# Kernel optimization log

Hardware: AMD Instinct MI355X
Metric: run time of the kernel (lower is better)

The kernel has to match this reference:

```python
import jax, jax.numpy as jnp
import numpy as np

DIM = 1536
DEPTH = 8
HEADS = 8
KV_HEADS = 1
GROUPS = HEADS // KV_HEADS
DQK = 128
DV = 192
DIM_PW = 128
POOL = 16
FF_INNER = int(DIM * 2.0)
SOFTCLAMP = 5.0
SCALE = 64 ** -0.5  # source uses default dim_head=64 for scale, not dim_head_qk
MAX_POS = 8192
EPS = float(jnp.finfo(jnp.float32).eps)


def rmsnorm(x, g):
    return x * jax.lax.rsqrt(jnp.mean(x * x, axis=-1, keepdims=True) + EPS) * g


def rotate_half(x):
    x1, x2 = jnp.split(x, 2, axis=-1)
    return jnp.concatenate([-x2, x1], axis=-1)


def apply_rope(pos, t):
    return t * jnp.cos(pos) + rotate_half(t) * jnp.sin(pos)


def rotary_emb(seq_len):
    nf = DQK // 2
    # torch.logspace(1, MAX_POS-nf+1, nf) = 10**linspace -> overflows to inf in fp32 (faithful)
    inv_freq = 1.0 / (jnp.arange(nf, dtype=jnp.float32) + 10.0 ** jnp.linspace(1.0, MAX_POS - nf + 1, nf, dtype=jnp.float32))
    freqs = jnp.arange(seq_len, dtype=jnp.float32)[:, None] * inv_freq[None, :]
    return jnp.concatenate([freqs, freqs], axis=-1)  # [n, DQK]


def softclamp(t, value=SOFTCLAMP):
    return jnp.tanh(t / value) * value


def attention(x, pairwise, rope, w_qkv, qg, kg, vg, bg, w_bias, w_out):
    b, n, _ = x.shape
    qkv = x @ w_qkv
    q, k, v = jnp.split(qkv, [HEADS * DQK, HEADS * DQK + DQK], axis=-1)
    # b n (g h d) -> b g h n d
    q = q.reshape(b, n, GROUPS, KV_HEADS, DQK).transpose(0, 2, 3, 1, 4)
    k = k.reshape(b, n, KV_HEADS, DQK).transpose(0, 2, 1, 3)
    v = v.reshape(b, n, KV_HEADS, DV).transpose(0, 2, 1, 3)
    q = rmsnorm(q, qg)
    k = rmsnorm(k, kg)
    v = rmsnorm(v, vg)
    q = q * SCALE
    q = apply_rope(rope, q)
    k = apply_rope(rope, k)
    sim = jnp.einsum('bghid,bhjd->bghij', q, k)
    # pairwise bias: RMSNorm -> GELU -> Linear(dim_pw, heads) -> b g h i j
    pb = jax.nn.gelu(rmsnorm(pairwise, bg), approximate=False) @ w_bias  # [b, i, j, heads]
    bi = pb.shape[1]
    bias = pb.reshape(b, bi, bi, GROUPS, KV_HEADS).transpose(0, 3, 4, 1, 2)
    bias = jnp.repeat(jnp.repeat(bias, POOL, axis=3), POOL, axis=4)  # expand to seq res
    sim = softclamp(sim + bias)
    attn = jax.nn.softmax(sim, axis=-1)
    out = jnp.einsum('bghij,bhjd->bghid', attn, v)
    out = out.transpose(0, 3, 1, 2, 4).reshape(b, n, GROUPS * KV_HEADS * DV)
    return out @ w_out


def tower(x, pairwise, w_qkv, q_gamma, k_gamma, v_gamma, bias_gamma, w_bias, w_out, attn_pre_gamma, ff_pre_gamma, w_ff1, b_ff1, w_ff2, b_ff2):
    rope = rotary_emb(x.shape[1])
    for d in range(DEPTH):
        xn = rmsnorm(x, attn_pre_gamma[d])
        x = x + attention(xn, pairwise, rope, w_qkv[d], q_gamma[d], k_gamma[d], v_gamma[d], bias_gamma[d], w_bias[d], w_out[d])
        xn = rmsnorm(x, ff_pre_gamma[d])
        x = x + (jax.nn.relu(xn @ w_ff1[d] + b_ff1[d]) @ w_ff2[d] + b_ff2[d])
    return x


def setup_inputs() -> dict:
    key = jax.random.key(0)
    ks = jax.random.split(key, 10)
    s = 0.02
    inp = {
        'x': jax.random.normal(ks[0], (2, 2048, DIM), jnp.float32),
        'pairwise': jax.random.normal(ks[1], (2, 128, 128, DIM_PW), jnp.float32),
        'w_qkv': jax.random.normal(ks[2], (DEPTH, DIM, HEADS * DQK + DQK + DV), jnp.float32) * s,
        'q_gamma': jnp.ones((DEPTH, DQK), jnp.float32),
        'k_gamma': jnp.ones((DEPTH, DQK), jnp.float32),
        'v_gamma': jnp.ones((DEPTH, DV), jnp.float32),
        'bias_gamma': jnp.ones((DEPTH, DIM_PW), jnp.float32),
        'w_bias': jax.random.normal(ks[3], (DEPTH, DIM_PW, HEADS), jnp.float32) * s,
        'w_out': jax.random.normal(ks[4], (DEPTH, DV * HEADS, DIM), jnp.float32) * s,
        'attn_pre_gamma': jnp.ones((DEPTH, DIM), jnp.float32),
        'ff_pre_gamma': jnp.ones((DEPTH, DIM), jnp.float32),
        'w_ff1': jax.random.normal(ks[5], (DEPTH, DIM, FF_INNER), jnp.float32) * s,
        'b_ff1': jnp.zeros((DEPTH, FF_INNER), jnp.float32),
        'w_ff2': jax.random.normal(ks[6], (DEPTH, FF_INNER, DIM), jnp.float32) * s,
        'b_ff2': jnp.zeros((DEPTH, DIM), jnp.float32),
    }
    return inp


def reference(x, pairwise, w_qkv, q_gamma, k_gamma, v_gamma, bias_gamma, w_bias, w_out, attn_pre_gamma, ff_pre_gamma, w_ff1, b_ff1, w_ff2, b_ff2):
    return tower(x, pairwise, w_qkv, q_gamma, k_gamma, v_gamma, bias_gamma, w_bias, w_out, attn_pre_gamma, ff_pre_gamma, w_ff1, b_ff1, w_ff2, b_ff2)
```

## Files before the change

kernel.cpp:

```cpp
#include <hip/hip_runtime.h>

typedef __bf16 bf16;
typedef float f32x4 __attribute__((ext_vector_type(4)));
typedef __bf16 bf16x8 __attribute__((ext_vector_type(8)));
typedef __bf16 bf16x4 __attribute__((ext_vector_type(4)));

#define EPSF 1.1920928955078125e-07f

#define GLOAD_LDS16(gsrc, ldst) \
  __builtin_amdgcn_global_load_lds((const __attribute__((address_space(1))) void*)(gsrc), \
                                   (__attribute__((address_space(3))) void*)(ldst), 16, 0, 0)

__device__ __forceinline__ float wave_reduce_sum(float v) {
#pragma unroll
  for (int m = 1; m < 64; m <<= 1) v += __shfl_xor(v, m, 64);
  return v;
}

__global__ __launch_bounds__(256) void wcast_t(const float* __restrict__ src,
                                               bf16* __restrict__ dst, int R, int C) {
  __shared__ float t[32][33];
  int z = blockIdx.z;
  const float* s = src + (size_t)z * R * C;
  bf16* d = dst + (size_t)z * R * C;
  int c0 = blockIdx.x * 32, r0 = blockIdx.y * 32;
  int tx = threadIdx.x, ty = threadIdx.y;
#pragma unroll
  for (int k = 0; k < 4; ++k)
    t[ty + k * 8][tx] = s[(size_t)(r0 + ty + k * 8) * C + c0 + tx];
  __syncthreads();
#pragma unroll
  for (int k = 0; k < 4; ++k)
    d[(size_t)(c0 + ty + k * 8) * R + r0 + tx] = (bf16)t[tx][ty + k * 8];
}

__global__ __launch_bounds__(256) void rmsnorm_k(const float* __restrict__ X,
                                                 const float* __restrict__ G,
                                                 bf16* __restrict__ O) {
  int row = blockIdx.x, tid = threadIdx.x, lane = tid & 63, w = tid >> 6;
  const float* x = X + (size_t)row * 1536;
  float v[6];
  float ss = 0.f;
#pragma unroll
  for (int k = 0; k < 6; ++k) { v[k] = x[tid + k * 256]; ss += v[k] * v[k]; }
  ss = wave_reduce_sum(ss);
  __shared__ float wsum[4];
  if (lane == 0) wsum[w] = ss;
  __syncthreads();
  ss = wsum[0] + wsum[1] + wsum[2] + wsum[3];
  float rs = rsqrtf(ss * (1.f / 1536.f) + EPSF);
  bf16* o = O + (size_t)row * 1536;
#pragma unroll
  for (int k = 0; k < 6; ++k) o[tid + k * 256] = (bf16)(v[k] * rs * G[tid + k * 256]);
}

template <int EPI>
__global__ __launch_bounds__(256, 3) void gemm_bt(const bf16* __restrict__ A,
                                                  const bf16* __restrict__ Bt,
                                                  float* __restrict__ Cf,
                                                  bf16* __restrict__ Cb,
                                                  const float* __restrict__ bias,
                                                  int M, int N, int K) {
  __shared__ __align__(16) char As[128 * 128];
  __shared__ __align__(16) char Bs[128 * 128];
  const int tid = threadIdx.x;
  const int lane = tid & 63, l15 = lane & 15, l4 = lane >> 4;
  const int w = tid >> 6;
  const int nwg = gridDim.x * gridDim.y;
  const int bid = blockIdx.y * gridDim.x + blockIdx.x;
  const int cpx = nwg >> 3;
  const int swz = (bid & 7) * cpx + (bid >> 3);
  const int rm = (swz / gridDim.x) * 128;
  const int cn = (swz % gridDim.x) * 128;
  const int wm = (w >> 1) * 64, wn = (w & 1) * 64;
  f32x4 acc[4][4] = {};

  for (int kk = 0; kk < K; kk += 64) {
#pragma unroll
    for (int r = 0; r < 4; ++r) {
      uint32_t o = (uint32_t)(r * 256 + tid) * 16;
      uint32_t row = o >> 7;
      uint32_t kb = ((o >> 4) & 7) ^ (row & 7);
      const bf16* src = A + (size_t)(rm + (int)row) * K + kk + kb * 8;
      GLOAD_LDS16(src, As + (o & 0xFFFFFC00u));
    }
#pragma unroll
    for (int r = 0; r < 4; ++r) {
      uint32_t o = (uint32_t)(r * 256 + tid) * 16;
      uint32_t row = o >> 7;
      uint32_t kb = ((o >> 4) & 7) ^ (row & 7);
      int nrow = cn + (int)row;
      if (nrow >= N) nrow = N - 1;
      const bf16* src = Bt + (size_t)nrow * K + kk + kb * 8;
      GLOAD_LDS16(src, Bs + (o & 0xFFFFFC00u));
    }
    __syncthreads();
#pragma unroll
    for (int s = 0; s < 2; ++s) {
      bf16x8 a[4], b[4];
#pragma unroll
      for (int m = 0; m < 4; ++m) {
        uint32_t row = wm + m * 16 + l15;
        uint32_t kb = (uint32_t)(s * 4 + l4);
        a[m] = *(const bf16x8*)(As + row * 128 + (kb ^ (row & 7)) * 16);
      }
#pragma unroll
      for (int n = 0; n < 4; ++n) {
        uint32_t row = wn + n * 16 + l15;
        uint32_t kb = (uint32_t)(s * 4 + l4);
        b[n] = *(const bf16x8*)(Bs + row * 128 + (kb ^ (row & 7)) * 16);
      }
      __builtin_amdgcn_s_setprio(1);
#pragma unroll
      for (int m = 0; m < 4; ++m)
#pragma unroll
        for (int n = 0; n < 4; ++n)
          acc[m][n] = __builtin_amdgcn_mfma_f32_16x16x32_bf16(a[m], b[n], acc[m][n], 0, 0, 0);
      __builtin_amdgcn_s_setprio(0);
    }
    __syncthreads();
  }

#pragma unroll
  for (int m = 0; m < 4; ++m)
#pragma unroll
    for (int n = 0; n < 4; ++n)
#pragma unroll
      for (int r = 0; r < 4; ++r) {
        int row = rm + wm + m * 16 + l4 * 4 + r;
        int col = cn + wn + n * 16 + l15;
        if (col < N) {
          float v = acc[m][n][r];
          size_t idx = (size_t)row * N + col;
          if constexpr (EPI == 0) {
            Cf[idx] = v;
          } else if constexpr (EPI == 2) {
            Cf[idx] += v;
          } else if constexpr (EPI == 3) {
            float tv = v + bias[col];
            Cb[idx] = (bf16)(tv > 0.f ? tv : 0.f);
          } else if constexpr (EPI == 4) {
            Cf[idx] += v + bias[col];
          }
        }
      }
}

template <int EPI>
__global__ __launch_bounds__(256, 4) void gemm_bt64(const bf16* __restrict__ A,
                                                    const bf16* __restrict__ Bt,
                                                    float* __restrict__ Cf,
                                                    bf16* __restrict__ Cb,
                                                    const float* __restrict__ bias,
                                                    int M, int N, int K) {
  __shared__ __align__(16) char As[64 * 128];
  __shared__ __align__(16) char Bs[128 * 128];
  const int tid = threadIdx.x;
  const int lane = tid & 63, l15 = lane & 15, l4 = lane >> 4;
  const int w = tid >> 6;
  const int nwg = gridDim.x * gridDim.y;
  const int bid = blockIdx.y * gridDim.x + blockIdx.x;
  const int cpx = nwg >> 3;
  const int swz = (bid & 7) * cpx + (bid >> 3);
  const int rm = (swz / gridDim.x) * 64;
  const int cn = (swz % gridDim.x) * 128;
  const int wm = (w >> 1) * 32, wn = (w & 1) * 64;
  f32x4 acc[2][4] = {};

  for (int kk = 0; kk < K; kk += 64) {
#pragma unroll
    for (int r = 0; r < 2; ++r) {
      uint32_t o = (uint32_t)(r * 256 + tid) * 16;
      uint32_t row = o >> 7;
      uint32_t kb = ((o >> 4) & 7) ^ (row & 7);
      const bf16* src = A + (size_t)(rm + (int)row) * K + kk + kb * 8;
      GLOAD_LDS16(src, As + (o & 0xFFFFFC00u));
    }
#pragma unroll
    for (int r = 0; r < 4; ++r) {
      uint32_t o = (uint32_t)(r * 256 + tid) * 16;
      uint32_t row = o >> 7;
      uint32_t kb = ((o >> 4) & 7) ^ (row & 7);
      int nrow = cn + (int)row;
      if (nrow >= N) nrow = N - 1;
      const bf16* src = Bt + (size_t)nrow * K + kk + kb * 8;
      GLOAD_LDS16(src, Bs + (o & 0xFFFFFC00u));
    }
    __syncthreads();
#pragma unroll
    for (int s = 0; s < 2; ++s) {
      bf16x8 a[2], b[4];
#pragma unroll
      for (int m = 0; m < 2; ++m) {
        uint32_t row = wm + m * 16 + l15;
        uint32_t kb = (uint32_t)(s * 4 + l4);
        a[m] = *(const bf16x8*)(As + row * 128 + (kb ^ (row & 7)) * 16);
      }
#pragma unroll
      for (int n = 0; n < 4; ++n) {
        uint32_t row = wn + n * 16 + l15;
        uint32_t kb = (uint32_t)(s * 4 + l4);
        b[n] = *(const bf16x8*)(Bs + row * 128 + (kb ^ (row & 7)) * 16);
      }
      __builtin_amdgcn_s_setprio(1);
#pragma unroll
      for (int m = 0; m < 2; ++m)
#pragma unroll
        for (int n = 0; n < 4; ++n)
          acc[m][n] = __builtin_amdgcn_mfma_f32_16x16x32_bf16(a[m], b[n], acc[m][n], 0, 0, 0);
      __builtin_amdgcn_s_setprio(0);
    }
    __syncthreads();
  }

#pragma unroll
  for (int m = 0; m < 2; ++m)
#pragma unroll
    for (int n = 0; n < 4; ++n)
#pragma unroll
      for (int r = 0; r < 4; ++r) {
        int row = rm + wm + m * 16 + l4 * 4 + r;
        int col = cn + wn + n * 16 + l15;
        if (col < N) {
          float v = acc[m][n][r];
          size_t idx = (size_t)row * N + col;
          if constexpr (EPI == 0) {
            Cf[idx] = v;
          } else if constexpr (EPI == 2) {
            Cf[idx] += v;
          } else if constexpr (EPI == 3) {
            float tv = v + bias[col];
            Cb[idx] = (bf16)(tv > 0.f ? tv : 0.f);
          } else if constexpr (EPI == 4) {
            Cf[idx] += v + bias[col];
          }
        }
      }
}

__global__ void qkv_post(const float* __restrict__ qkv, const float* __restrict__ qg,
                         const float* __restrict__ kg, const float* __restrict__ vg,
                         bf16* __restrict__ Qo, bf16* __restrict__ Ko, bf16* __restrict__ Vo) {
  int t = blockIdx.x, seg = blockIdx.y, lane = threadIdx.x;
  int b = t >> 11, n = t & 2047;
  const float* base;
  const float* gamma;
  int len;
  if (seg < 8) { base = qkv + (size_t)t * 1344 + seg * 128; gamma = qg; len = 128; }
  else if (seg == 8) { base = qkv + (size_t)t * 1344 + 1024; gamma = kg; len = 128; }
  else { base = qkv + (size_t)t * 1344 + 1152; gamma = vg; len = 192; }
  float v0 = base[lane], v1 = base[lane + 64];
  float v2 = (len == 192) ? base[lane + 128] : 0.f;
  float ss = wave_reduce_sum(v0 * v0 + v1 * v1 + v2 * v2);
  float rs = rsqrtf(ss / (float)len + EPSF);
  float n0 = v0 * rs * gamma[lane];
  float n1 = v1 * rs * gamma[lane + 64];
  if (seg < 8) {
    n0 *= 0.125f; n1 *= 0.125f;
    if (lane == 0) {
      float th = 0.1f * (float)n;
      float c = cosf(th), s_ = sinf(th);
      float r0 = n0 * c - n1 * s_, r1 = n1 * c + n0 * s_;
      n0 = r0; n1 = r1;
    }
    bf16* q = Qo + ((size_t)((b * 8 + seg) * 2048 + n)) * 128;
    q[lane] = (bf16)n0; q[lane + 64] = (bf16)n1;
  } else if (seg == 8) {
    if (lane == 0) {
      float th = 0.1f * (float)n;
      float c = cosf(th), s_ = sinf(th);
      float r0 = n0 * c - n1 * s_, r1 = n1 * c + n0 * s_;
      n0 = r0; n1 = r1;
    }
    bf16* k = Ko + ((size_t)(b * 2048 + n)) * 128;
    k[lane] = (bf16)n0; k[lane + 64] = (bf16)n1;
  } else {
    float n2 = v2 * rs * vg[lane + 128];
    bf16* vp = Vo + ((size_t)(b * 2048 + n)) * 192;
    vp[lane] = (bf16)n0; vp[lane + 64] = (bf16)n1; vp[lane + 128] = (bf16)n2;
  }
}

__global__ __launch_bounds__(256) void vtrans(const bf16* __restrict__ V, bf16* __restrict__ Vt) {
  __shared__ bf16 t[32][33];
  int b = blockIdx.z;
  int j0 = blockIdx.x * 32, d0 = blockIdx.y * 32;
  int tx = threadIdx.x, ty = threadIdx.y;
#pragma unroll
  for (int k = 0; k < 4; ++k)
    t[ty + k * 8][tx] = V[((size_t)b * 2048 + j0 + ty + k * 8) * 192 + d0 + tx];
  __syncthreads();
#pragma unroll
  for (int k = 0; k < 4; ++k)
    Vt[((size_t)b * 192 + d0 + ty + k * 8) * 2048 + j0 + tx] = t[tx][ty + k * 8];
}

__global__ void bias_pw(const float* __restrict__ P, const float* __restrict__ g,
                        const float* __restrict__ Wb, float* __restrict__ Bout) {
  int j = blockIdx.x, i = blockIdx.y, b = blockIdx.z;
  int lane = threadIdx.x;
  const float* p = P + (((size_t)b * 128 + i) * 128 + j) * 128;
  float a0 = p[lane], a1 = p[lane + 64];
  float ss = wave_reduce_sum(a0 * a0 + a1 * a1);
  float rs = rsqrtf(ss * (1.f / 128.f) + EPSF);
  float x0 = a0 * rs * g[lane], x1 = a1 * rs * g[lane + 64];
  float g0 = 0.5f * x0 * (1.f + erff(x0 * 0.70710678118654752f));
  float g1 = 0.5f * x1 * (1.f + erff(x1 * 0.70710678118654752f));
  __shared__ float gs[128];
  gs[lane] = g0; gs[lane + 64] = g1;
  __syncthreads();
  int h = lane & 7;
  float acc = 0.f;
#pragma unroll
  for (int k = 0; k < 16; ++k) {
    int c = (lane >> 3) + k * 8;
    acc += gs[c] * Wb[c * 8 + h];
  }
  acc += __shfl_xor(acc, 8, 64);
  acc += __shfl_xor(acc, 16, 64);
  acc += __shfl_xor(acc, 32, 64);
  if (lane < 8) Bout[(((size_t)b * 8 + lane) * 128 + i) * 128 + j] = acc;
}

__global__ __launch_bounds__(256, 3) void attn_k(const bf16* __restrict__ Q,
                                                 const bf16* __restrict__ Kg,
                                                 const bf16* __restrict__ Vt,
                                                 const float* __restrict__ Bias,
                                                 bf16* __restrict__ Out) {
  __shared__ __align__(16) char Ks[64 * 256];
  __shared__ __align__(16) char Vs[192 * 128];
  __shared__ __align__(16) char Ps[64 * 128];
  __shared__ float BiasS[4 * 128];
  int tid = threadIdx.x, lane = tid & 63, w = tid >> 6;
  int it = blockIdx.x, g = blockIdx.y, b = blockIdx.z;
  int i0 = it * 64;
  int l15 = lane & 15, l4 = lane >> 4;

  bf16x8 qf[4];
#pragma unroll
  for (int s = 0; s < 4; ++s)
    qf[s] = *(const bf16x8*)(Q + ((size_t)((b * 8 + g) * 2048 + i0 + w * 16 + l15)) * 128 + s * 32 + l4 * 8);

  if (tid < 128) {
    int r = tid >> 5, c = (tid & 31) * 4;
    float4 bv = *(const float4*)(Bias + ((size_t)((b * 8 + g) * 128) + (i0 >> 4) + r) * 128 + c);
    bv.x *= 0.57707801635558535f; bv.y *= 0.57707801635558535f;
    bv.z *= 0.57707801635558535f; bv.w *= 0.57707801635558535f;
    *(float4*)&BiasS[r * 128 + c] = bv;
  }

  f32x4 accO[12] = {};
  float lacc = 0.f;

  for (int jt = 0; jt < 32; ++jt) {
    int j0 = jt * 64;
#pragma unroll
    for (int r = 0; r < 4; ++r) {
      uint32_t o = (uint32_t)(r * 256 + tid) * 16;
      uint32_t row = o >> 8;
      uint32_t kb = ((o >> 4) & 15) ^ (row & 15);
      const bf16* src = Kg + ((size_t)b * 2048 + j0 + (int)row) * 128 + kb * 8;
      GLOAD_LDS16(src, Ks + (o & 0xFFFFFC00u));
    }
#pragma unroll
    for (int r = 0; r < 6; ++r) {
      uint32_t o = (uint32_t)(r * 256 + tid) * 16;
      uint32_t dv = o >> 7;
      uint32_t kb = ((o >> 4) & 7) ^ (dv & 7);
      const bf16* src = Vt + ((size_t)b * 192 + dv) * 2048 + j0 + kb * 8;
      GLOAD_LDS16(src, Vs + (o & 0xFFFFFC00u));
    }
    __syncthreads();

    f32x4 accS[4] = {};
#pragma unroll
    for (int s = 0; s < 4; ++s) {
      bf16x8 kf[4];
#pragma unroll
      for (int n = 0; n < 4; ++n) {
        uint32_t row = n * 16 + l15;
        uint32_t kb = (uint32_t)(s * 4 + l4);
        kf[n] = *(const bf16x8*)(Ks + row * 256 + (kb ^ (row & 15)) * 16);
      }
      __builtin_amdgcn_s_setprio(1);
#pragma unroll
      for (int n = 0; n < 4; ++n)
        accS[n] = __builtin_amdgcn_mfma_f32_16x16x32_bf16(kf[n], qf[s], accS[n], 0, 0, 0);
      __builtin_amdgcn_s_setprio(0);
    }

#pragma unroll
    for (int n = 0; n < 4; ++n) {
      float biaS = BiasS[w * 128 + jt * 4 + n];
      bf16x4 pk;
#pragma unroll
      for (int r = 0; r < 4; ++r) {
        float t1 = __builtin_fmaf(0.57707801635558535f, accS[n][r], biaS);
        float e1 = exp2f(t1);
        float rr = __builtin_amdgcn_rcpf(e1 + 1.0f);
        float pv = exp2f(-14.426950408889634f * rr);
        lacc += pv;
        pk[r] = (bf16)pv;
      }
      uint32_t prow = (uint32_t)(w * 16 + l15);
      uint32_t byteo = prow * 128 + (uint32_t)(n * 16 + l4 * 4) * 2;
      byteo ^= (prow & 7) << 4;
      *(bf16x4*)(Ps + byteo) = pk;
    }

#pragma unroll
    for (int s = 0; s < 2; ++s) {
      uint32_t prow = (uint32_t)(w * 16 + l15);
      uint32_t byteo = prow * 128 + (uint32_t)(s * 64 + l4 * 16);
      byteo ^= (prow & 7) << 4;
      bf16x8 pa = *(const bf16x8*)(Ps + byteo);
#pragma unroll
      for (int n = 0; n < 12; ++n) {
        uint32_t dvr = n * 16 + l15;
        uint32_t kb = (uint32_t)(s * 4 + l4);
        bf16x8 vf = *(const bf16x8*)(Vs + dvr * 128 + (kb ^ (dvr & 7)) * 16);
        __builtin_amdgcn_s_setprio(1);
        accO[n] = __builtin_amdgcn_mfma_f32_16x16x32_bf16(vf, pa, accO[n], 0, 0, 0);
        __builtin_amdgcn_s_setprio(0);
      }
    }
    __syncthreads();
  }

  lacc += __shfl_xor(lacc, 16, 64);
  lacc += __shfl_xor(lacc, 32, 64);
  float rl = __builtin_amdgcn_rcpf(lacc);

  {
    int i = i0 + w * 16 + l15;
#pragma unroll
    for (int n = 0; n < 12; ++n) {
      bf16x4 ok;
#pragma unroll
      for (int r = 0; r < 4; ++r) ok[r] = (bf16)(accO[n][r] * rl);
      int dv = n * 16 + l4 * 4;
      *(bf16x4*)(Out + ((size_t)(b * 2048 + i)) * 1536 + g * 192 + dv) = ok;
    }
  }
}

extern "C" void kernel_launch(void* const* d_in, const int* in_sizes, int n_in,
                              void* d_out, int out_size, void* d_ws, size_t ws_size,
                              hipStream_t stream) {
  (void)in_sizes; (void)n_in; (void)out_size;
  const float* x_in = (const float*)d_in[0];
  const float* pairwise = (const float*)d_in[1];
  const float* w_qkv = (const float*)d_in[2];
  const float* q_gamma = (const float*)d_in[3];
  const float* k_gamma = (const float*)d_in[4];
  const float* v_gamma = (const float*)d_in[5];
  const float* bias_gamma = (const float*)d_in[6];
  const float* w_bias = (const float*)d_in[7];
  const float* w_out = (const float*)d_in[8];
  const float* attn_pre = (const float*)d_in[9];
  const float* ff_pre = (const float*)d_in[10];
  const float* w_ff1 = (const float*)d_in[11];
  const float* b_ff1 = (const float*)d_in[12];
  const float* w_ff2 = (const float*)d_in[13];
  const float* b_ff2 = (const float*)d_in[14];

  char* p = (char*)d_ws;
  auto alloc = [&](size_t bytes) {
    char* r = p;
    p += (bytes + 255) & ~(size_t)255;
    return r;
  };
  bf16* wT_qkv = (bf16*)alloc(8ull * 1344 * 1536 * 2);
  bf16* wT_out = (bf16*)alloc(8ull * 1536 * 1536 * 2);
  bf16* wT_ff1 = (bf16*)alloc(8ull * 3072 * 1536 * 2);
  bf16* wT_ff2 = (bf16*)alloc(8ull * 1536 * 3072 * 2);
  float* x_ws = (float*)alloc(4096ull * 1536 * 4);
  bf16* xn = (bf16*)alloc(4096ull * 1536 * 2);
  float* qkvb = (float*)alloc(4096ull * 1344 * 4);
  bf16* qb = (bf16*)alloc(2ull * 8 * 2048 * 128 * 2);
  bf16* kb = (bf16*)alloc(2ull * 2048 * 128 * 2);
  bf16* vb = (bf16*)alloc(2ull * 2048 * 192 * 2);
  bf16* vtb = (bf16*)alloc(2ull * 192 * 2048 * 2);
  float* biasb = (float*)alloc(2ull * 8 * 128 * 128 * 4);
  bf16* attn_o = (bf16*)alloc(4096ull * 1536 * 2);
  bf16* hb = (bf16*)alloc(4096ull * 3072 * 2);
  if ((size_t)(p - (char*)d_ws) > ws_size) return;

  wcast_t<<<dim3(42, 48, 8), dim3(32, 8), 0, stream>>>(w_qkv, wT_qkv, 1536, 1344);
  wcast_t<<<dim3(48, 48, 8), dim3(32, 8), 0, stream>>>(w_out, wT_out, 1536, 1536);
  wcast_t<<<dim3(96, 48, 8), dim3(32, 8), 0, stream>>>(w_ff1, wT_ff1, 1536, 3072);
  wcast_t<<<dim3(48, 96, 8), dim3(32, 8), 0, stream>>>(w_ff2, wT_ff2, 3072, 1536);

  hipMemcpyAsync(x_ws, x_in, 4096ull * 1536 * 4, hipMemcpyDeviceToDevice, stream);

  for (int d = 0; d < 8; ++d) {
    const bf16* wq = wT_qkv + (size_t)d * 1344 * 1536;
    const bf16* wo = wT_out + (size_t)d * 1536 * 1536;
    const bf16* w1 = wT_ff1 + (size_t)d * 3072 * 1536;
    const bf16* w2 = wT_ff2 + (size_t)d * 1536 * 3072;

    rmsnorm_k<<<4096, 256, 0, stream>>>(x_ws, attn_pre + d * 1536, xn);
    gemm_bt64<0><<<dim3(11, 64), 256, 0, stream>>>(xn, wq, qkvb, nullptr, nullptr, 4096, 1344, 1536);
    qkv_post<<<dim3(4096, 10), 64, 0, stream>>>(qkvb, q_gamma + d * 128, k_gamma + d * 128,
                                                v_gamma + d * 192, qb, kb, vb);
    vtrans<<<dim3(64, 6, 2), dim3(32, 8), 0, stream>>>(vb, vtb);
    bias_pw<<<dim3(128, 128, 2), 64, 0, stream>>>(pairwise, bias_gamma + d * 128,
                                                  w_bias + d * 128 * 8, biasb);
    attn_k<<<dim3(32, 8, 2), 256, 0, stream>>>(qb, kb, vtb, biasb, attn_o);
    gemm_bt64<2><<<dim3(12, 64), 256, 0, stream>>>(attn_o, wo, x_ws, nullptr, nullptr, 4096, 1536, 1536);
    rmsnorm_k<<<4096, 256, 0, stream>>>(x_ws, ff_pre + d * 1536, xn);
    gemm_bt<3><<<dim3(24, 32), 256, 0, stream>>>(xn, w1, nullptr, hb, b_ff1 + d * 3072, 4096, 3072, 1536);
    gemm_bt64<4><<<dim3(12, 64), 256, 0, stream>>>(hb, w2, x_ws, nullptr, b_ff2 + d * 1536, 4096, 1536, 3072);
  }

  hipMemcpyAsync(d_out, x_ws, 4096ull * 1536 * 4, hipMemcpyDeviceToDevice, stream);
}
```

Baseline: 2.475 ms.

## Load GEMM A operand directly from global memory and emit bf16 QKV output

Both GEMM kernels stop staging the A tile through LDS. Each wave now reads its A fragments straight from global memory in the MFMA loop, which removes the A shared-memory traffic and frees LDS for higher occupancy. The cost is uncoalesced, unreused global reads that now sit on the MFMA critical path. Separately, the QKV projection writes bf16 instead of fp32, roughly halving the intermediate's write and read traffic, and qkv_post is updated to read bf16.

```diff
diff --git a/kernel.cpp b/kernel.cpp
--- a/kernel.cpp
+++ b/kernel.cpp
@@ -61,7 +61,6 @@
                                                   bf16* __restrict__ Cb,
                                                   const float* __restrict__ bias,
                                                   int M, int N, int K) {
-  __shared__ __align__(16) char As[128 * 128];
   __shared__ __align__(16) char Bs[128 * 128];
   const int tid = threadIdx.x;
   const int lane = tid & 63, l15 = lane & 15, l4 = lane >> 4;
@@ -81,14 +80,6 @@
       uint32_t o = (uint32_t)(r * 256 + tid) * 16;
       uint32_t row = o >> 7;
       uint32_t kb = ((o >> 4) & 7) ^ (row & 7);
-      const bf16* src = A + (size_t)(rm + (int)row) * K + kk + kb * 8;
-      GLOAD_LDS16(src, As + (o & 0xFFFFFC00u));
-    }
-#pragma unroll
-    for (int r = 0; r < 4; ++r) {
-      uint32_t o = (uint32_t)(r * 256 + tid) * 16;
-      uint32_t row = o >> 7;
-      uint32_t kb = ((o >> 4) & 7) ^ (row & 7);
       int nrow = cn + (int)row;
       if (nrow >= N) nrow = N - 1;
       const bf16* src = Bt + (size_t)nrow * K + kk + kb * 8;
@@ -99,11 +90,8 @@
     for (int s = 0; s < 2; ++s) {
       bf16x8 a[4], b[4];
 #pragma unroll
-      for (int m = 0; m < 4; ++m) {
-        uint32_t row = wm + m * 16 + l15;
-        uint32_t kb = (uint32_t)(s * 4 + l4);
-        a[m] = *(const bf16x8*)(As + row * 128 + (kb ^ (row & 7)) * 16);
-      }
+      for (int m = 0; m < 4; ++m)
+        a[m] = *(const bf16x8*)(A + (size_t)(rm + wm + m * 16 + l15) * K + kk + (s * 4 + l4) * 8);
 #pragma unroll
       for (int n = 0; n < 4; ++n) {
         uint32_t row = wn + n * 16 + l15;
@@ -132,15 +120,15 @@
         if (col < N) {
           float v = acc[m][n][r];
           size_t idx = (size_t)row * N + col;
-          if constexpr (EPI == 0) {
-            Cf[idx] = v;
-          } else if constexpr (EPI == 2) {
+          if constexpr (EPI == 2) {
             Cf[idx] += v;
           } else if constexpr (EPI == 3) {
             float tv = v + bias[col];
             Cb[idx] = (bf16)(tv > 0.f ? tv : 0.f);
           } else if constexpr (EPI == 4) {
             Cf[idx] += v + bias[col];
+          } else if constexpr (EPI == 5) {
+            Cb[idx] = (bf16)v;
           }
         }
       }
@@ -153,7 +141,6 @@
                                                     bf16* __restrict__ Cb,
                                                     const float* __restrict__ bias,
                                                     int M, int N, int K) {
-  __shared__ __align__(16) char As[64 * 128];
   __shared__ __align__(16) char Bs[128 * 128];
   const int tid = threadIdx.x;
   const int lane = tid & 63, l15 = lane & 15, l4 = lane >> 4;
@@ -169,14 +156,6 @@
 
   for (int kk = 0; kk < K; kk += 64) {
 #pragma unroll
-    for (int r = 0; r < 2; ++r) {
-      uint32_t o = (uint32_t)(r * 256 + tid) * 16;
-      uint32_t row = o >> 7;
-      uint32_t kb = ((o >> 4) & 7) ^ (row & 7);
-      const bf16* src = A + (size_t)(rm + (int)row) * K + kk + kb * 8;
-      GLOAD_LDS16(src, As + (o & 0xFFFFFC00u));
-    }
-#pragma unroll
     for (int r = 0; r < 4; ++r) {
       uint32_t o = (uint32_t)(r * 256 + tid) * 16;
       uint32_t row = o >> 7;
@@ -191,11 +170,8 @@
     for (int s = 0; s < 2; ++s) {
       bf16x8 a[2], b[4];
 #pragma unroll
-      for (int m = 0; m < 2; ++m) {
-        uint32_t row = wm + m * 16 + l15;
-        uint32_t kb = (uint32_t)(s * 4 + l4);
-        a[m] = *(const bf16x8*)(As + row * 128 + (kb ^ (row & 7)) * 16);
-      }
+      for (int m = 0; m < 2; ++m)
+        a[m] = *(const bf16x8*)(A + (size_t)(rm + wm + m * 16 + l15) * K + kk + (s * 4 + l4) * 8);
 #pragma unroll
       for (int n = 0; n < 4; ++n) {
         uint32_t row = wn + n * 16 + l15;
@@ -224,33 +200,33 @@
         if (col < N) {
           float v = acc[m][n][r];
           size_t idx = (size_t)row * N + col;
-          if constexpr (EPI == 0) {
-            Cf[idx] = v;
-          } else if constexpr (EPI == 2) {
+          if constexpr (EPI == 2) {
             Cf[idx] += v;
           } else if constexpr (EPI == 3) {
             float tv = v + bias[col];
             Cb[idx] = (bf16)(tv > 0.f ? tv : 0.f);
           } else if constexpr (EPI == 4) {
             Cf[idx] += v + bias[col];
+          } else if constexpr (EPI == 5) {
+            Cb[idx] = (bf16)v;
           }
         }
       }
 }
 
-__global__ void qkv_post(const float* __restrict__ qkv, const float* __restrict__ qg,
+__global__ void qkv_post(const bf16* __restrict__ qkv, const float* __restrict__ qg,
                          const float* __restrict__ kg, const float* __restrict__ vg,
                          bf16* __restrict__ Qo, bf16* __restrict__ Ko, bf16* __restrict__ Vo) {
   int t = blockIdx.x, seg = blockIdx.y, lane = threadIdx.x;
   int b = t >> 11, n = t & 2047;
-  const float* base;
+  const bf16* base;
   const float* gamma;
   int len;
   if (seg < 8) { base = qkv + (size_t)t * 1344 + seg * 128; gamma = qg; len = 128; }
   else if (seg == 8) { base = qkv + (size_t)t * 1344 + 1024; gamma = kg; len = 128; }
   else { base = qkv + (size_t)t * 1344 + 1152; gamma = vg; len = 192; }
-  float v0 = base[lane], v1 = base[lane + 64];
-  float v2 = (len == 192) ? base[lane + 128] : 0.f;
+  float v0 = (float)base[lane], v1 = (float)base[lane + 64];
+  float v2 = (len == 192) ? (float)base[lane + 128] : 0.f;
   float ss = wave_reduce_sum(v0 * v0 + v1 * v1 + v2 * v2);
   float rs = rsqrtf(ss / (float)len + EPSF);
   float n0 = v0 * rs * gamma[lane];
@@ -476,7 +452,7 @@
   bf16* wT_ff2 = (bf16*)alloc(8ull * 1536 * 3072 * 2);
   float* x_ws = (float*)alloc(4096ull * 1536 * 4);
   bf16* xn = (bf16*)alloc(4096ull * 1536 * 2);
-  float* qkvb = (float*)alloc(4096ull * 1344 * 4);
+  bf16* qkvb = (bf16*)alloc(4096ull * 1344 * 2);
   bf16* qb = (bf16*)alloc(2ull * 8 * 2048 * 128 * 2);
   bf16* kb = (bf16*)alloc(2ull * 2048 * 128 * 2);
   bf16* vb = (bf16*)alloc(2ull * 2048 * 192 * 2);
@@ -500,7 +476,7 @@
     const bf16* w2 = wT_ff2 + (size_t)d * 1536 * 3072;
 
     rmsnorm_k<<<4096, 256, 0, stream>>>(x_ws, attn_pre + d * 1536, xn);
-    gemm_bt64<0><<<dim3(11, 64), 256, 0, stream>>>(xn, wq, qkvb, nullptr, nullptr, 4096, 1344, 1536);
+    gemm_bt64<5><<<dim3(11, 64), 256, 0, stream>>>(xn, wq, nullptr, qkvb, nullptr, 4096, 1344, 1536);
     qkv_post<<<dim3(4096, 10), 64, 0, stream>>>(qkvb, q_gamma + d * 128, k_gamma + d * 128,
                                                 v_gamma + d * 192, qb, kb, vb);
     vtrans<<<dim3(64, 6, 2), dim3(32, 8), 0, stream>>>(vb, vtb);
```

Result: slower. 3.493 ms (+41.2%).
